# Performance work log

Measured on AMD Instinct MI355X. Metric: run time of the kernel, lower is better.

Reference implementation:

```python
import jax, jax.numpy as jnp
import numpy as np

N, C, HI, WI = 8, 3, 512, 512   # src_img NCHW (input_img_size)
HO, WO = 2048, 2048             # output canvas (output_img_size[2:])
EPS = 1e-8


def _transform_one(img, coor_row):
    """Replicates: sigmoid box params -> theta -> F.affine_grid -> F.grid_sample
    (bilinear, zeros padding, align_corners=False). Theta has zero off-diagonals,
    so the grid is separable in x/y and the bilinear sample factorizes.
    img: [C, HI, WI]; coor_row: [4]. Returns (sample [C,HO,WO], mask [HO,WO])."""
    x = jax.nn.sigmoid(coor_row[0]) * WO
    y = jax.nn.sigmoid(coor_row[1]) * HO
    w = jax.nn.sigmoid(coor_row[2]) * WO
    h = jax.nn.sigmoid(coor_row[3]) * HO
    a = WO / (w + EPS)
    tx = 2.0 / WO * (WO / 2.0 - x) * a
    b = HO / (h + EPS)
    ty = 2.0 / HO * (HO / 2.0 - y) * b
    # affine_grid base coords (align_corners=False): center-of-pixel normalized
    xs = (2.0 * jnp.arange(WO, dtype=img.dtype) + 1.0) / WO - 1.0
    ys = (2.0 * jnp.arange(HO, dtype=img.dtype) + 1.0) / HO - 1.0
    gx = a * xs + tx          # [WO]
    gy = b * ys + ty          # [HO]
    # grid_sample unnormalize (align_corners=False)
    ix = ((gx + 1.0) * WI - 1.0) / 2.0
    iy = ((gy + 1.0) * HI - 1.0) / 2.0
    x0f = jnp.floor(ix); y0f = jnp.floor(iy)
    wx1 = ix - x0f; wx0 = 1.0 - wx1
    wy1 = iy - y0f; wy0 = 1.0 - wy1
    x0 = x0f.astype(jnp.int32); x1 = x0 + 1
    y0 = y0f.astype(jnp.int32); y1 = y0 + 1
    vx0 = ((x0 >= 0) & (x0 < WI)).astype(img.dtype)
    vx1 = ((x1 >= 0) & (x1 < WI)).astype(img.dtype)
    vy0 = ((y0 >= 0) & (y0 < HI)).astype(img.dtype)
    vy1 = ((y1 >= 0) & (y1 < HI)).astype(img.dtype)
    x0c = jnp.clip(x0, 0, WI - 1); x1c = jnp.clip(x1, 0, WI - 1)
    y0c = jnp.clip(y0, 0, HI - 1); y1c = jnp.clip(y1, 0, HI - 1)
    wyv0 = wy0 * vy0; wyv1 = wy1 * vy1
    wxv0 = wx0 * vx0; wxv1 = wx1 * vx1
    # separable bilinear gather with zero padding
    rows = img[:, y0c, :] * wyv0[None, :, None] + img[:, y1c, :] * wyv1[None, :, None]  # [C,HO,WI]
    samp = rows[:, :, x0c] * wxv0[None, None, :] + rows[:, :, x1c] * wxv1[None, None, :]  # [C,HO,WO]
    # grid_sample of an all-ones mask == sum of in-bounds bilinear weights (separable)
    mask = (wyv0 + wyv1)[:, None] * (wxv0 + wxv1)[None, :]  # [HO,WO]
    return samp, mask


def _composite(src_img, bg_img, coor):
    def step(bg, inp):
        img, c = inp
        s, m = _transform_one(img, c)
        bg = bg * (1.0 - m)[None, None] + (s * m[None])[None]
        return bg, None
    bg, _ = jax.lax.scan(step, bg_img, (src_img, coor))
    return bg


def setup_inputs() -> dict:
    key = jax.random.key(0)
    k1, k2, k3 = jax.random.split(key, 3)
    src_img = jax.random.normal(k1, (N, C, HI, WI), dtype=jnp.float32)
    bg_img = jax.random.uniform(k2, (1, C, HO, WO), dtype=jnp.float32)
    coor = jax.random.normal(k3, (N, 4), dtype=jnp.float32)  # nn.Parameter
    return {"src_img": src_img, "bg_img": bg_img, "coor": coor}


def reference(src_img, bg_img, coor):
    return _composite(src_img, bg_img, coor)
```

## Files before the change

kernel.cpp:

```cpp
#include <hip/hip_runtime.h>

#define WI 512
#define HI 512
#define WO 2048
#define HO 2048
#define NIMG 8
#define CCH 3
#define EPS 1e-8f
#define PLANE (HI * WI)

#define TPB  256
#define SEG  1024
#define PXT  4

__launch_bounds__(TPB)
__global__ void diffcomp_v12(const float* __restrict__ src,
                             const float* __restrict__ bg,
                             const float* __restrict__ coor,
                             float* __restrict__ out) {
    __shared__ float4 stY[NIMG];
    __shared__ float4 stX[NIMG];

    const int tid = threadIdx.x;
    const int b0  = blockIdx.x;
    const int b   = ((b0 & 7) << 9) | (b0 >> 3);
    const int row = b >> 1;
    const int wo0 = (b & 1) << 10;
    const float ys  = (2.0f * (float)row + 1.0f) / (float)HO - 1.0f;
    const float HW1 = 0.5f * (float)(WI - 1);

    if (tid < NIMG) {
        const float cx  = coor[tid * 4 + 0];
        const float cy  = coor[tid * 4 + 1];
        const float cw  = coor[tid * 4 + 2];
        const float chh = coor[tid * 4 + 3];
        const float xx = (1.0f / (1.0f + expf(-cx))) * (float)WO;
        const float yy = (1.0f / (1.0f + expf(-cy))) * (float)HO;
        const float w  = (1.0f / (1.0f + expf(-cw))) * (float)WO;
        const float h  = (1.0f / (1.0f + expf(-chh))) * (float)HO;
        const float a  = (float)WO / (w + EPS);
        const float bb = (float)HO / (h + EPS);
        const float ty = (2.0f / (float)HO) * ((float)HO * 0.5f - yy) * bb;

        const float gy  = bb * ys + ty;
        const float iy  = ((gy + 1.0f) * (float)HI - 1.0f) * 0.5f;
        const float y0f = floorf(iy);
        const float fy1 = iy - y0f;
        const float fy0 = 1.0f - fy1;
        const float y1f = y0f + 1.0f;
        const float v0  = (y0f >= 0.0f && y0f < (float)HI) ? 1.0f : 0.0f;
        const float v1  = (y1f >= 0.0f && y1f < (float)HI) ? 1.0f : 0.0f;
        const float wy0 = fy0 * v0;
        const float wy1 = fy1 * v1;
        const float my  = wy0 + wy1;
        const float y0of = fminf(fmaxf(y0f, 0.0f), (float)(HI - 1)) * (float)WI;
        const float y1of = fminf(fmaxf(y1f, 0.0f), (float)(HI - 1)) * (float)WI;

        const float A2 = a * ((float)WI / (float)WO);
        const float D  = 0.5f - xx;

        float validf = 0.0f;
        if (my > 0.0f) {
            const float ixf = fmaf(A2, (float)wo0 + D, HW1);
            const float ixl = fmaf(A2, (float)(wo0 + SEG - 1) + D, HW1);
            if (!(ixl <= -1.0f || ixf >= (float)WI)) validf = 1.0f;
        }
        stY[tid] = make_float4(wy0, wy1, y0of, y1of);
        stX[tid] = make_float4(A2, D, my, validf);
    }
    __syncthreads();

    const int pw0 = wo0 + ((tid >> 6) << 8);
    unsigned wvis = 0u, wintr = 0u;
    int jw = -1;
#pragma unroll
    for (int n = 0; n < NIMG; n++) {
        const float4 SX = stX[n];
        if (SX.w > 0.0f) {
            const float ixF = fmaf(SX.x, (float)pw0 + SX.y, HW1);
            const float ixL = fmaf(SX.x, (float)(pw0 + 255) + SX.y, HW1);
            if (!(ixL <= -1.0f || ixF >= (float)WI)) {
                wvis |= (1u << n);
                if (ixF >= 0.0f && ixL < (float)(WI - 1)) {
                    wintr |= (1u << n);
                    if (SX.z == 1.0f) jw = n;
                }
            }
        }
    }
    if (jw >= 0) wvis &= ~((1u << jw) - 1u);

    const int px0   = wo0 + (tid << 2);
    const int gbase = row * WO + px0;

    float acc[CCH][PXT];
    if (jw < 0) {
#pragma unroll
        for (int c = 0; c < CCH; c++) {
            const float4 bv = *(const float4*)&bg[c * (HO * WO) + gbase];
            acc[c][0] = bv.x; acc[c][1] = bv.y; acc[c][2] = bv.z; acc[c][3] = bv.w;
        }
    } else {
#pragma unroll
        for (int c = 0; c < CCH; c++)
#pragma unroll
            for (int p = 0; p < PXT; p++)
                acc[c][p] = 0.0f;
    }

    float xpf[PXT];
#pragma unroll
    for (int p = 0; p < PXT; p++) xpf[p] = (float)(px0 + p);

    while (wvis) {
        const int n = (int)__builtin_ctz(wvis);
        wvis &= wvis - 1u;
        const float4 SX = stX[n];
        const float4 SY = stY[n];
        const float A2 = SX.x, Dv = SX.y, my = SX.z;
        const float wy0 = SY.x, wy1 = SY.y;
        const int y0o = (int)SY.z;
        const int y1o = (int)SY.w;
        const float* ib = src + n * (CCH * PLANE);

        if ((wintr >> n) & 1u) {
            const float omy = 1.0f - my;
            if (omy == 0.0f) {
#pragma unroll
                for (int p = 0; p < PXT; p++) {
                    const float ix  = fmaf(A2, xpf[p] + Dv, HW1);
                    const float x0f = floorf(ix);
                    const float fx1 = ix - x0f;
                    const int   k   = (int)x0f;
                    const float* p0 = ib + y0o + k;
                    const float* p1 = ib + y1o + k;
#pragma unroll
                    for (int c = 0; c < CCH; c++) {
                        const float r00 = p0[c * PLANE];
                        const float r01 = p0[c * PLANE + 1];
                        const float r10 = p1[c * PLANE];
                        const float r11 = p1[c * PLANE + 1];
                        const float q0 = r00 * wy0 + r10 * wy1;
                        const float q1 = r01 * wy0 + r11 * wy1;
                        acc[c][p] = q0 + fx1 * (q1 - q0);
                    }
                }
            } else {
#pragma unroll
                for (int p = 0; p < PXT; p++) {
                    const float ix  = fmaf(A2, xpf[p] + Dv, HW1);
                    const float x0f = floorf(ix);
                    const float fx1 = ix - x0f;
                    const int   k   = (int)x0f;
                    const float* p0 = ib + y0o + k;
                    const float* p1 = ib + y1o + k;
#pragma unroll
                    for (int c = 0; c < CCH; c++) {
                        const float r00 = p0[c * PLANE];
                        const float r01 = p0[c * PLANE + 1];
                        const float r10 = p1[c * PLANE];
                        const float r11 = p1[c * PLANE + 1];
                        const float q0 = r00 * wy0 + r10 * wy1;
                        const float q1 = r01 * wy0 + r11 * wy1;
                        const float sc = q0 + fx1 * (q1 - q0);
                        acc[c][p] = acc[c][p] * omy + my * sc;
                    }
                }
            }
        } else {
#pragma unroll
            for (int p = 0; p < PXT; p++) {
                const float ix  = fmaf(A2, xpf[p] + Dv, HW1);
                const float x0f = floorf(ix);
                const float fx1 = ix - x0f;
                const float fx0 = 1.0f - fx1;
                const float x1f = x0f + 1.0f;
                const float v0  = (x0f >= 0.0f && x0f < (float)WI) ? 1.0f : 0.0f;
                const float v1  = (x1f >= 0.0f && x1f < (float)WI) ? 1.0f : 0.0f;
                const float wx0 = fx0 * v0;
                const float wx1 = fx1 * v1;
                const int x0c = (int)fminf(fmaxf(x0f, 0.0f), (float)(WI - 1));
                const int x1c = (int)fminf(fmaxf(x1f, 0.0f), (float)(WI - 1));
                const float m  = my * (wx0 + wx1);
                const float om = 1.0f - m;
#pragma unroll
                for (int c = 0; c < CCH; c++) {
                    const float* cb = ib + c * PLANE;
                    const float q00 = cb[y0o + x0c];
                    const float q10 = cb[y1o + x0c];
                    const float q01 = cb[y0o + x1c];
                    const float q11 = cb[y1o + x1c];
                    const float q0 = q00 * wy0 + q10 * wy1;
                    const float q1 = q01 * wy0 + q11 * wy1;
                    const float sc = q0 * wx0 + q1 * wx1;
                    acc[c][p] = acc[c][p] * om + sc * m;
                }
            }
        }
    }

#pragma unroll
    for (int c = 0; c < CCH; c++)
        *(float4*)&out[c * (HO * WO) + gbase] =
            make_float4(acc[c][0], acc[c][1], acc[c][2], acc[c][3]);
}

extern "C" void kernel_launch(void* const* d_in, const int* in_sizes, int n_in,
                              void* d_out, int out_size, void* d_ws, size_t ws_size,
                              hipStream_t stream) {
    const float* src  = (const float*)d_in[0];
    const float* bg   = (const float*)d_in[1];
    const float* coor = (const float*)d_in[2];
    float* out = (float*)d_out;
    (void)d_ws; (void)ws_size;

    hipLaunchKernelGGL(diffcomp_v12, dim3(HO * (WO / SEG)), dim3(TPB), 0, stream,
                       src, bg, coor, out);
}
```

Baseline: 142.9 us.

## Process four row-segments per workgroup to amortize per-block setup

Each workgroup now covers two output rows (four 1024-pixel segments) instead of one segment, computing the per-image sigmoid/affine parameters once and storing per-row y-weights in shared memory. This cuts the block count by four and amortizes the coordinate setup, the shared-memory fill and the barrier. It also adds a min-blocks hint to launch bounds. The trade-off is fewer workgroups for latency hiding, a larger unrolled body and more register pressure, and the segment loop is sequential within a thread.

```diff
diff --git a/kernel.cpp b/kernel.cpp
--- a/kernel.cpp
+++ b/kernel.cpp
@@ -12,21 +12,22 @@
 #define TPB  256
 #define SEG  1024
 #define PXT  4
-
-__launch_bounds__(TPB)
-__global__ void diffcomp_v12(const float* __restrict__ src,
+#define SEGS 4
+#define NWG  (HO * (WO / SEG) / SEGS)
+
+__launch_bounds__(TPB, 4)
+__global__ void diffcomp_v13(const float* __restrict__ src,
                              const float* __restrict__ bg,
                              const float* __restrict__ coor,
                              float* __restrict__ out) {
-    __shared__ float4 stY[NIMG];
-    __shared__ float4 stX[NIMG];
+    __shared__ float4 stA[NIMG];
+    __shared__ float4 stY[2][NIMG];
 
     const int tid = threadIdx.x;
-    const int b0  = blockIdx.x;
-    const int b   = ((b0 & 7) << 9) | (b0 >> 3);
-    const int row = b >> 1;
-    const int wo0 = (b & 1) << 10;
-    const float ys  = (2.0f * (float)row + 1.0f) / (float)HO - 1.0f;
+    const int wg0 = blockIdx.x;
+    const int wg  = ((wg0 & 7) << 7) | (wg0 >> 3);
+    const int segbase = wg << 2;
+    const int row0 = segbase >> 1;
     const float HW1 = 0.5f * (float)(WI - 1);
 
     if (tid < NIMG) {
@@ -42,167 +43,174 @@
         const float bb = (float)HO / (h + EPS);
         const float ty = (2.0f / (float)HO) * ((float)HO * 0.5f - yy) * bb;
 
-        const float gy  = bb * ys + ty;
-        const float iy  = ((gy + 1.0f) * (float)HI - 1.0f) * 0.5f;
-        const float y0f = floorf(iy);
-        const float fy1 = iy - y0f;
-        const float fy0 = 1.0f - fy1;
-        const float y1f = y0f + 1.0f;
-        const float v0  = (y0f >= 0.0f && y0f < (float)HI) ? 1.0f : 0.0f;
-        const float v1  = (y1f >= 0.0f && y1f < (float)HI) ? 1.0f : 0.0f;
-        const float wy0 = fy0 * v0;
-        const float wy1 = fy1 * v1;
-        const float my  = wy0 + wy1;
-        const float y0of = fminf(fmaxf(y0f, 0.0f), (float)(HI - 1)) * (float)WI;
-        const float y1of = fminf(fmaxf(y1f, 0.0f), (float)(HI - 1)) * (float)WI;
-
         const float A2 = a * ((float)WI / (float)WO);
         const float D  = 0.5f - xx;
 
-        float validf = 0.0f;
-        if (my > 0.0f) {
-            const float ixf = fmaf(A2, (float)wo0 + D, HW1);
-            const float ixl = fmaf(A2, (float)(wo0 + SEG - 1) + D, HW1);
-            if (!(ixl <= -1.0f || ixf >= (float)WI)) validf = 1.0f;
-        }
-        stY[tid] = make_float4(wy0, wy1, y0of, y1of);
-        stX[tid] = make_float4(A2, D, my, validf);
+        float myv[2];
+#pragma unroll
+        for (int r = 0; r < 2; r++) {
+            const float ys  = (2.0f * (float)(row0 + r) + 1.0f) / (float)HO - 1.0f;
+            const float gy  = bb * ys + ty;
+            const float iy  = ((gy + 1.0f) * (float)HI - 1.0f) * 0.5f;
+            const float y0f = floorf(iy);
+            const float fy1 = iy - y0f;
+            const float fy0 = 1.0f - fy1;
+            const float y1f = y0f + 1.0f;
+            const float v0  = (y0f >= 0.0f && y0f < (float)HI) ? 1.0f : 0.0f;
+            const float v1  = (y1f >= 0.0f && y1f < (float)HI) ? 1.0f : 0.0f;
+            const float wy0 = fy0 * v0;
+            const float wy1 = fy1 * v1;
+            myv[r] = wy0 + wy1;
+            const float y0of = fminf(fmaxf(y0f, 0.0f), (float)(HI - 1)) * (float)WI;
+            const float y1of = fminf(fmaxf(y1f, 0.0f), (float)(HI - 1)) * (float)WI;
+            stY[r][tid] = make_float4(wy0, wy1, y0of, y1of);
+        }
+        stA[tid] = make_float4(A2, D, myv[0], myv[1]);
     }
     __syncthreads();
 
-    const int pw0 = wo0 + ((tid >> 6) << 8);
-    unsigned wvis = 0u, wintr = 0u;
-    int jw = -1;
-#pragma unroll
-    for (int n = 0; n < NIMG; n++) {
-        const float4 SX = stX[n];
-        if (SX.w > 0.0f) {
-            const float ixF = fmaf(SX.x, (float)pw0 + SX.y, HW1);
-            const float ixL = fmaf(SX.x, (float)(pw0 + 255) + SX.y, HW1);
-            if (!(ixL <= -1.0f || ixF >= (float)WI)) {
-                wvis |= (1u << n);
-                if (ixF >= 0.0f && ixL < (float)(WI - 1)) {
-                    wintr |= (1u << n);
-                    if (SX.z == 1.0f) jw = n;
+#pragma unroll
+    for (int s = 0; s < SEGS; s++) {
+        const int row = row0 + (s >> 1);
+        const int rp  = s >> 1;
+        const int wo0 = (s & 1) << 10;
+
+        const int pw0 = wo0 + ((tid >> 6) << 8);
+        unsigned wvis = 0u, wintr = 0u;
+        int jw = -1;
+#pragma unroll
+        for (int n = 0; n < NIMG; n++) {
+            const float4 SA = stA[n];
+            const float myn = rp ? SA.w : SA.z;
+            if (myn > 0.0f) {
+                const float ixF = fmaf(SA.x, (float)pw0 + SA.y, HW1);
+                const float ixL = fmaf(SA.x, (float)(pw0 + 255) + SA.y, HW1);
+                if (!(ixL <= -1.0f || ixF >= (float)WI)) {
+                    wvis |= (1u << n);
+                    if (ixF >= 0.0f && ixL < (float)(WI - 1)) {
+                        wintr |= (1u << n);
+                        if (myn == 1.0f) jw = n;
+                    }
                 }
             }
         }
-    }
-    if (jw >= 0) wvis &= ~((1u << jw) - 1u);
-
-    const int px0   = wo0 + (tid << 2);
-    const int gbase = row * WO + px0;
-
-    float acc[CCH][PXT];
-    if (jw < 0) {
-#pragma unroll
-        for (int c = 0; c < CCH; c++) {
-            const float4 bv = *(const float4*)&bg[c * (HO * WO) + gbase];
-            acc[c][0] = bv.x; acc[c][1] = bv.y; acc[c][2] = bv.z; acc[c][3] = bv.w;
-        }
-    } else {
-#pragma unroll
-        for (int c = 0; c < CCH; c++)
-#pragma unroll
-            for (int p = 0; p < PXT; p++)
-                acc[c][p] = 0.0f;
-    }
-
-    float xpf[PXT];
-#pragma unroll
-    for (int p = 0; p < PXT; p++) xpf[p] = (float)(px0 + p);
-
-    while (wvis) {
-        const int n = (int)__builtin_ctz(wvis);
-        wvis &= wvis - 1u;
-        const float4 SX = stX[n];
-        const float4 SY = stY[n];
-        const float A2 = SX.x, Dv = SX.y, my = SX.z;
-        const float wy0 = SY.x, wy1 = SY.y;
-        const int y0o = (int)SY.z;
-        const int y1o = (int)SY.w;
-        const float* ib = src + n * (CCH * PLANE);
-
-        if ((wintr >> n) & 1u) {
-            const float omy = 1.0f - my;
-            if (omy == 0.0f) {
+        if (jw >= 0) wvis &= ~((1u << jw) - 1u);
+
+        const int px0   = wo0 + (tid << 2);
+        const int gbase = row * WO + px0;
+
+        float acc[CCH][PXT];
+        if (jw < 0) {
+#pragma unroll
+            for (int c = 0; c < CCH; c++) {
+                const float4 bv = *(const float4*)&bg[c * (HO * WO) + gbase];
+                acc[c][0] = bv.x; acc[c][1] = bv.y; acc[c][2] = bv.z; acc[c][3] = bv.w;
+            }
+        } else {
+#pragma unroll
+            for (int c = 0; c < CCH; c++)
+#pragma unroll
+                for (int p = 0; p < PXT; p++)
+                    acc[c][p] = 0.0f;
+        }
+
+        float xpf[PXT];
+#pragma unroll
+        for (int p = 0; p < PXT; p++) xpf[p] = (float)(px0 + p);
+
+        while (wvis) {
+            const int n = (int)__builtin_ctz(wvis);
+            wvis &= wvis - 1u;
+            const float4 SA = stA[n];
+            const float4 SY = stY[rp][n];
+            const float A2 = SA.x, Dv = SA.y;
+            const float my = rp ? SA.w : SA.z;
+            const float wy0 = SY.x, wy1 = SY.y;
+            const int y0o = (int)SY.z;
+            const int y1o = (int)SY.w;
+            const float* ib = src + n * (CCH * PLANE);
+
+            if ((wintr >> n) & 1u) {
+                const float omy = 1.0f - my;
+                if (omy == 0.0f) {
+#pragma unroll
+                    for (int p = 0; p < PXT; p++) {
+                        const float ix  = fmaf(A2, xpf[p] + Dv, HW1);
+                        const float x0f = floorf(ix);
+                        const float fx1 = ix - x0f;
+                        const int   k   = (int)x0f;
+                        const float* p0 = ib + y0o + k;
+                        const float* p1 = ib + y1o + k;
+#pragma unroll
+                        for (int c = 0; c < CCH; c++) {
+                            const float r00 = p0[c * PLANE];
+                            const float r01 = p0[c * PLANE + 1];
+                            const float r10 = p1[c * PLANE];
+                            const float r11 = p1[c * PLANE + 1];
+                            const float q0 = r00 * wy0 + r10 * wy1;
+                            const float q1 = r01 * wy0 + r11 * wy1;
+                            acc[c][p] = q0 + fx1 * (q1 - q0);
+                        }
+                    }
+                } else {
+#pragma unroll
+                    for (int p = 0; p < PXT; p++) {
+                        const float ix  = fmaf(A2, xpf[p] + Dv, HW1);
+                        const float x0f = floorf(ix);
+                        const float fx1 = ix - x0f;
+                        const int   k   = (int)x0f;
+                        const float* p0 = ib + y0o + k;
+                        const float* p1 = ib + y1o + k;
+#pragma unroll
+                        for (int c = 0; c < CCH; c++) {
+                            const float r00 = p0[c * PLANE];
+                            const float r01 = p0[c * PLANE + 1];
+                            const float r10 = p1[c * PLANE];
+                            const float r11 = p1[c * PLANE + 1];
+                            const float q0 = r00 * wy0 + r10 * wy1;
+                            const float q1 = r01 * wy0 + r11 * wy1;
+                            const float sc = q0 + fx1 * (q1 - q0);
+                            acc[c][p] = acc[c][p] * omy + my * sc;
+                        }
+                    }
+                }
+            } else {
 #pragma unroll
                 for (int p = 0; p < PXT; p++) {
                     const float ix  = fmaf(A2, xpf[p] + Dv, HW1);
                     const float x0f = floorf(ix);
                     const float fx1 = ix - x0f;
-                    const int   k   = (int)x0f;
-                    const float* p0 = ib + y0o + k;
-                    const float* p1 = ib + y1o + k;
+                    const float fx0 = 1.0f - fx1;
+                    const float x1f = x0f + 1.0f;
+                    const float v0  = (x0f >= 0.0f && x0f < (float)WI) ? 1.0f : 0.0f;
+                    const float v1  = (x1f >= 0.0f && x1f < (float)WI) ? 1.0f : 0.0f;
+                    const float wx0 = fx0 * v0;
+                    const float wx1 = fx1 * v1;
+                    const int x0c = (int)fminf(fmaxf(x0f, 0.0f), (float)(WI - 1));
+                    const int x1c = (int)fminf(fmaxf(x1f, 0.0f), (float)(WI - 1));
+                    const float m  = my * (wx0 + wx1);
+                    const float om = 1.0f - m;
 #pragma unroll
                     for (int c = 0; c < CCH; c++) {
-                        const float r00 = p0[c * PLANE];
-                        const float r01 = p0[c * PLANE + 1];
-                        const float r10 = p1[c * PLANE];
-                        const float r11 = p1[c * PLANE + 1];
-                        const float q0 = r00 * wy0 + r10 * wy1;
-                        const float q1 = r01 * wy0 + r11 * wy1;
-                        acc[c][p] = q0 + fx1 * (q1 - q0);
-                    }
-                }
-            } else {
-#pragma unroll
-                for (int p = 0; p < PXT; p++) {
-                    const float ix  = fmaf(A2, xpf[p] + Dv, HW1);
-                    const float x0f = floorf(ix);
-                    const float fx1 = ix - x0f;
-                    const int   k   = (int)x0f;
-                    const float* p0 = ib + y0o + k;
-                    const float* p1 = ib + y1o + k;
-#pragma unroll
-                    for (int c = 0; c < CCH; c++) {
-                        const float r00 = p0[c * PLANE];
-                        const float r01 = p0[c * PLANE + 1];
-                        const float r10 = p1[c * PLANE];
-                        const float r11 = p1[c * PLANE + 1];
-                        const float q0 = r00 * wy0 + r10 * wy1;
-                        const float q1 = r01 * wy0 + r11 * wy1;
-                        const float sc = q0 + fx1 * (q1 - q0);
-                        acc[c][p] = acc[c][p] * omy + my * sc;
+                        const float* cb = ib + c * PLANE;
+                        const float q00 = cb[y0o + x0c];
+                        const float q10 = cb[y1o + x0c];
+                        const float q01 = cb[y0o + x1c];
+                        const float q11 = cb[y1o + x1c];
+                        const float q0 = q00 * wy0 + q10 * wy1;
+                        const float q1 = q01 * wy0 + q11 * wy1;
+                        const float sc = q0 * wx0 + q1 * wx1;
+                        acc[c][p] = acc[c][p] * om + sc * m;
                     }
                 }
             }
-        } else {
-#pragma unroll
-            for (int p = 0; p < PXT; p++) {
-                const float ix  = fmaf(A2, xpf[p] + Dv, HW1);
-                const float x0f = floorf(ix);
-                const float fx1 = ix - x0f;
-                const float fx0 = 1.0f - fx1;
-                const float x1f = x0f + 1.0f;
-                const float v0  = (x0f >= 0.0f && x0f < (float)WI) ? 1.0f : 0.0f;
-                const float v1  = (x1f >= 0.0f && x1f < (float)WI) ? 1.0f : 0.0f;
-                const float wx0 = fx0 * v0;
-                const float wx1 = fx1 * v1;
-                const int x0c = (int)fminf(fmaxf(x0f, 0.0f), (float)(WI - 1));
-                const int x1c = (int)fminf(fmaxf(x1f, 0.0f), (float)(WI - 1));
-                const float m  = my * (wx0 + wx1);
-                const float om = 1.0f - m;
-#pragma unroll
-                for (int c = 0; c < CCH; c++) {
-                    const float* cb = ib + c * PLANE;
-                    const float q00 = cb[y0o + x0c];
-                    const float q10 = cb[y1o + x0c];
-                    const float q01 = cb[y0o + x1c];
-                    const float q11 = cb[y1o + x1c];
-                    const float q0 = q00 * wy0 + q10 * wy1;
-                    const float q1 = q01 * wy0 + q11 * wy1;
-                    const float sc = q0 * wx0 + q1 * wx1;
-                    acc[c][p] = acc[c][p] * om + sc * m;
-                }
-            }
-        }
+        }
+
+#pragma unroll
+        for (int c = 0; c < CCH; c++)
+            *(float4*)&out[c * (HO * WO) + gbase] =
+                make_float4(acc[c][0], acc[c][1], acc[c][2], acc[c][3]);
     }
-
-#pragma unroll
-    for (int c = 0; c < CCH; c++)
-        *(float4*)&out[c * (HO * WO) + gbase] =
-            make_float4(acc[c][0], acc[c][1], acc[c][2], acc[c][3]);
 }
 
 extern "C" void kernel_launch(void* const* d_in, const int* in_sizes, int n_in,
@@ -214,6 +222,6 @@
     float* out = (float*)d_out;
     (void)d_ws; (void)ws_size;
 
-    hipLaunchKernelGGL(diffcomp_v12, dim3(HO * (WO / SEG)), dim3(TPB), 0, stream,
+    hipLaunchKernelGGL(diffcomp_v13, dim3(NWG), dim3(TPB), 0, stream,
                        src, bg, coor, out);
 }
```

Result: faster. 140.0 us (-2.0%).

## Stage vertically-interpolated source rows in per-wave LDS before horizontal sampling

Applied to the files above, without the earlier changes.

Each 64-lane wave now loads the needed span of the two source rows with coalesced float4 reads, does the vertical lerp once per source column, and stores the result interleaved by channel in a per-wave shared-memory slot. The horizontal lerp then reads from LDS, so scattered global gathers and repeated vertical blends across neighbouring output pixels are avoided. Blocks now cover a full output row with 512 threads instead of half a row with 256. The cost is about 50KB of LDS per block, which limits occupancy, plus a per-image staging pass. The code has no barrier between staging and reading; it relies on each slot being private to one wave.

```diff
diff --git a/kernel.cpp b/kernel.cpp
--- a/kernel.cpp
+++ b/kernel.cpp
@@ -9,24 +9,24 @@
 #define EPS 1e-8f
 #define PLANE (HI * WI)
 
-#define TPB  256
-#define SEG  1024
-#define PXT  4
+#define TPB   512
+#define NWAVE 8
+#define WPX   256
+#define PXT   4
+#define CAPW  520
 
 __launch_bounds__(TPB)
-__global__ void diffcomp_v12(const float* __restrict__ src,
+__global__ void diffcomp_v14(const float* __restrict__ src,
                              const float* __restrict__ bg,
                              const float* __restrict__ coor,
                              float* __restrict__ out) {
+    __shared__ __align__(16) float cs[NWAVE][CAPW * CCH];
+    __shared__ float4 stA[NIMG];
     __shared__ float4 stY[NIMG];
-    __shared__ float4 stX[NIMG];
 
     const int tid = threadIdx.x;
     const int b0  = blockIdx.x;
-    const int b   = ((b0 & 7) << 9) | (b0 >> 3);
-    const int row = b >> 1;
-    const int wo0 = (b & 1) << 10;
-    const float ys  = (2.0f * (float)row + 1.0f) / (float)HO - 1.0f;
+    const int row = ((b0 & 7) << 8) | (b0 >> 3);
     const float HW1 = 0.5f * (float)(WI - 1);
 
     if (tid < NIMG) {
@@ -42,6 +42,7 @@
         const float bb = (float)HO / (h + EPS);
         const float ty = (2.0f / (float)HO) * ((float)HO * 0.5f - yy) * bb;
 
+        const float ys  = (2.0f * (float)row + 1.0f) / (float)HO - 1.0f;
         const float gy  = bb * ys + ty;
         const float iy  = ((gy + 1.0f) * (float)HI - 1.0f) * 0.5f;
         const float y0f = floorf(iy);
@@ -59,39 +60,35 @@
         const float A2 = a * ((float)WI / (float)WO);
         const float D  = 0.5f - xx;
 
-        float validf = 0.0f;
-        if (my > 0.0f) {
-            const float ixf = fmaf(A2, (float)wo0 + D, HW1);
-            const float ixl = fmaf(A2, (float)(wo0 + SEG - 1) + D, HW1);
-            if (!(ixl <= -1.0f || ixf >= (float)WI)) validf = 1.0f;
-        }
-        stY[tid] = make_float4(wy0, wy1, y0of, y1of);
-        stX[tid] = make_float4(A2, D, my, validf);
+        stA[tid] = make_float4(A2, D, my, wy0);
+        stY[tid] = make_float4(wy1, y0of, y1of, 0.0f);
     }
     __syncthreads();
 
-    const int pw0 = wo0 + ((tid >> 6) << 8);
+    const int wid  = tid >> 6;
+    const int lane = tid & 63;
+    const int pw0  = wid << 8;
+    const int px0  = pw0 + (lane << 2);
+    const int gbase = row * WO + px0;
+
     unsigned wvis = 0u, wintr = 0u;
     int jw = -1;
 #pragma unroll
     for (int n = 0; n < NIMG; n++) {
-        const float4 SX = stX[n];
-        if (SX.w > 0.0f) {
-            const float ixF = fmaf(SX.x, (float)pw0 + SX.y, HW1);
-            const float ixL = fmaf(SX.x, (float)(pw0 + 255) + SX.y, HW1);
+        const float4 SA = stA[n];
+        if (SA.z > 0.0f) {
+            const float ixF = fmaf(SA.x, (float)pw0 + SA.y, HW1);
+            const float ixL = fmaf(SA.x, (float)(pw0 + WPX - 1) + SA.y, HW1);
             if (!(ixL <= -1.0f || ixF >= (float)WI)) {
                 wvis |= (1u << n);
                 if (ixF >= 0.0f && ixL < (float)(WI - 1)) {
                     wintr |= (1u << n);
-                    if (SX.z == 1.0f) jw = n;
+                    if (SA.z == 1.0f) jw = n;
                 }
             }
         }
     }
     if (jw >= 0) wvis &= ~((1u << jw) - 1u);
-
-    const int px0   = wo0 + (tid << 2);
-    const int gbase = row * WO + px0;
 
     float acc[CCH][PXT];
     if (jw < 0) {
@@ -112,17 +109,54 @@
 #pragma unroll
     for (int p = 0; p < PXT; p++) xpf[p] = (float)(px0 + p);
 
+    float* const slot = cs[wid];
+
     while (wvis) {
         const int n = (int)__builtin_ctz(wvis);
         wvis &= wvis - 1u;
-        const float4 SX = stX[n];
+        const float4 SA = stA[n];
         const float4 SY = stY[n];
-        const float A2 = SX.x, Dv = SX.y, my = SX.z;
-        const float wy0 = SY.x, wy1 = SY.y;
-        const int y0o = (int)SY.z;
-        const int y1o = (int)SY.w;
-        const float* ib = src + n * (CCH * PLANE);
-
+        const float A2 = SA.x, Dv = SA.y, my = SA.z;
+        const float wy0 = SA.w, wy1 = SY.x;
+        const int y0o = (int)SY.y;
+        const int y1o = (int)SY.z;
+
+        const float ixF = fmaf(A2, (float)pw0 + Dv, HW1);
+        const float ixL = fmaf(A2, (float)(pw0 + WPX - 1) + Dv, HW1);
+        const int t0  = (int)fminf(fmaxf(floorf(ixF), 0.0f), (float)(WI - 1));
+        const int t1  = (int)fminf(fmaxf(floorf(ixL) + 1.0f, 0.0f), (float)(WI - 1));
+        const int t0a = t0 & ~3;
+        int R = (t1 - t0a + 4) & ~3;
+        if (R > WI - t0a) R = WI - t0a;
+        const int lim = t1 - t0a;
+
+        const float* ib = src + n * (CCH * PLANE) + t0a;
+
+#pragma unroll
+        for (int sw = 0; sw < 2; sw++) {
+            const int xo = (lane << 2) + (sw << 8);
+            if (xo < R) {
+                float4 r0[CCH], r1[CCH];
+#pragma unroll
+                for (int c = 0; c < CCH; c++) {
+                    r0[c] = *(const float4*)(ib + c * PLANE + y0o + xo);
+                    r1[c] = *(const float4*)(ib + c * PLANE + y1o + xo);
+                }
+                float wv[12];
+#pragma unroll
+                for (int t = 0; t < 4; t++)
+#pragma unroll
+                    for (int c = 0; c < CCH; c++)
+                        wv[t * CCH + c] = ((const float*)&r0[c])[t] * wy0
+                                        + ((const float*)&r1[c])[t] * wy1;
+                float* dst = &slot[xo * CCH];
+                ((float4*)dst)[0] = make_float4(wv[0], wv[1], wv[2],  wv[3]);
+                ((float4*)dst)[1] = make_float4(wv[4], wv[5], wv[6],  wv[7]);
+                ((float4*)dst)[2] = make_float4(wv[8], wv[9], wv[10], wv[11]);
+            }
+        }
+
+        const float t0af = (float)t0a;
         if ((wintr >> n) & 1u) {
             const float omy = 1.0f - my;
             if (omy == 0.0f) {
@@ -131,17 +165,12 @@
                     const float ix  = fmaf(A2, xpf[p] + Dv, HW1);
                     const float x0f = floorf(ix);
                     const float fx1 = ix - x0f;
-                    const int   k   = (int)x0f;
-                    const float* p0 = ib + y0o + k;
-                    const float* p1 = ib + y1o + k;
+                    const int   k   = (int)(x0f - t0af);
+                    const float* tp = slot + k * CCH;
 #pragma unroll
                     for (int c = 0; c < CCH; c++) {
-                        const float r00 = p0[c * PLANE];
-                        const float r01 = p0[c * PLANE + 1];
-                        const float r10 = p1[c * PLANE];
-                        const float r11 = p1[c * PLANE + 1];
-                        const float q0 = r00 * wy0 + r10 * wy1;
-                        const float q1 = r01 * wy0 + r11 * wy1;
+                        const float q0 = tp[c];
+                        const float q1 = tp[c + CCH];
                         acc[c][p] = q0 + fx1 * (q1 - q0);
                     }
                 }
@@ -151,17 +180,12 @@
                     const float ix  = fmaf(A2, xpf[p] + Dv, HW1);
                     const float x0f = floorf(ix);
                     const float fx1 = ix - x0f;
-                    const int   k   = (int)x0f;
-                    const float* p0 = ib + y0o + k;
-                    const float* p1 = ib + y1o + k;
+                    const int   k   = (int)(x0f - t0af);
+                    const float* tp = slot + k * CCH;
 #pragma unroll
                     for (int c = 0; c < CCH; c++) {
-                        const float r00 = p0[c * PLANE];
-                        const float r01 = p0[c * PLANE + 1];
-                        const float r10 = p1[c * PLANE];
-                        const float r11 = p1[c * PLANE + 1];
-                        const float q0 = r00 * wy0 + r10 * wy1;
-                        const float q1 = r01 * wy0 + r11 * wy1;
+                        const float q0 = tp[c];
+                        const float q1 = tp[c + CCH];
                         const float sc = q0 + fx1 * (q1 - q0);
                         acc[c][p] = acc[c][p] * omy + my * sc;
                     }
@@ -179,21 +203,17 @@
                 const float v1  = (x1f >= 0.0f && x1f < (float)WI) ? 1.0f : 0.0f;
                 const float wx0 = fx0 * v0;
                 const float wx1 = fx1 * v1;
-                const int x0c = (int)fminf(fmaxf(x0f, 0.0f), (float)(WI - 1));
-                const int x1c = (int)fminf(fmaxf(x1f, 0.0f), (float)(WI - 1));
+                int x0r = (int)fminf(fmaxf(x0f, 0.0f), (float)(WI - 1)) - t0a;
+                int x1r = (int)fminf(fmaxf(x1f, 0.0f), (float)(WI - 1)) - t0a;
+                x0r = min(max(x0r, 0), lim);
+                x1r = min(max(x1r, 0), lim);
                 const float m  = my * (wx0 + wx1);
                 const float om = 1.0f - m;
 #pragma unroll
                 for (int c = 0; c < CCH; c++) {
-                    const float* cb = ib + c * PLANE;
-                    const float q00 = cb[y0o + x0c];
-                    const float q10 = cb[y1o + x0c];
-                    const float q01 = cb[y0o + x1c];
-                    const float q11 = cb[y1o + x1c];
-                    const float q0 = q00 * wy0 + q10 * wy1;
-                    const float q1 = q01 * wy0 + q11 * wy1;
-                    const float sc = q0 * wx0 + q1 * wx1;
-                    acc[c][p] = acc[c][p] * om + sc * m;
+                    const float q0 = slot[x0r * CCH + c];
+                    const float q1 = slot[x1r * CCH + c];
+                    acc[c][p] = acc[c][p] * om + (q0 * wx0 + q1 * wx1) * m;
                 }
             }
         }
@@ -214,6 +234,6 @@
     float* out = (float*)d_out;
     (void)d_ws; (void)ws_size;
 
-    hipLaunchKernelGGL(diffcomp_v12, dim3(HO * (WO / SEG)), dim3(TPB), 0, stream,
+    hipLaunchKernelGGL(diffcomp_v14, dim3(HO), dim3(TPB), 0, stream,
                        src, bg, coor, out);
 }
```

Result: faster. 127.5 us (-10.8%).
